# Kernel optimization log

Measured on AMD Instinct MI355X. Metric: run time of the kernel, lower is better.

The kernel has to match this reference:

```python
import jax, jax.numpy as jnp
import numpy as np
import math

EPS = 1e-8
NUM_FREQS = 64
NUM_BINS = 128
NUM_QUERIES = 32768
HEAD_DIM = NUM_FREQS * 2


def setup_inputs() -> dict:
    key = jax.random.key(0)
    k1, k2, k3, k4, k5 = jax.random.split(key, 5)
    init_value = math.log(math.e - 1.0)
    return {
        "Q": jax.random.normal(k1, (NUM_QUERIES, HEAD_DIM), dtype=jnp.float32),
        "rotated_probes": jax.random.normal(k2, (NUM_BINS, HEAD_DIM), dtype=jnp.float32),
        # faithful init is full(init_value); add small noise so grads are non-degenerate
        "q_weights_raw": init_value + 0.1 * jax.random.normal(k3, (NUM_BINS, NUM_FREQS), dtype=jnp.float32),
        "q_magnitude_weights": 0.1 * jax.random.normal(k4, (NUM_BINS, NUM_FREQS), dtype=jnp.float32),
        "q_bias": 0.1 * jax.random.normal(k5, (NUM_BINS,), dtype=jnp.float32),
    }


def reference(Q, rotated_probes, q_weights_raw, q_magnitude_weights, q_bias):
    F = NUM_FREQS
    # L2-normalize queries (use_l2_norm=True)
    Qn = Q / (jnp.linalg.norm(Q, axis=-1, keepdims=True) + EPS)  # (q, d)
    Q_real, Q_imag = Qn[:, :F], Qn[:, F:]                        # (q, f)
    P_real, P_imag = rotated_probes[:, :F], rotated_probes[:, F:]  # (b, f)
    # per-frequency complex error and distance: (q, b, f)
    error_real = P_real[None, :, :] - Q_real[:, None, :]
    error_imag = P_imag[None, :, :] - Q_imag[:, None, :]
    distance = jnp.sqrt(error_real ** 2 + error_imag ** 2 + EPS)
    # per-frequency magnitude of normalized Q: (q, f)
    Q_magnitude = jnp.sqrt(Q_real ** 2 + Q_imag ** 2 + EPS)
    # negative weights via softplus
    effective_weights = -jax.nn.softplus(q_weights_raw)          # (b, f)
    distance_term = jnp.einsum('qbf,bf->qb', distance, effective_weights)
    magnitude_term = Q_magnitude @ q_magnitude_weights.T          # (q, b)
    scores = distance_term + magnitude_term + q_bias[None, :]
    return scores
```

## Files before the change

### kernel.cpp

```cpp
#include <hip/hip_runtime.h>
#include <math.h>

#define NUM_FREQS   64
#define NUM_BINS    128
#define NUM_QUERIES 32768
#define HEAD_DIM    128
#define EPS         1e-8f
#define NQB         16

__global__ void prep_fused(const float* __restrict__ Q,
                           const float* __restrict__ rp,
                           const float* __restrict__ wraw,
                           const float* __restrict__ mw,
                           float2* __restrict__ Qri,
                           float*  __restrict__ Qm,
                           float4* __restrict__ probeA,
                           float*  __restrict__ probeM) {
    const int bid = blockIdx.x;
    const int tid = threadIdx.x;
    if (bid < 128) {
        int q = bid * 256 + tid;
        const float4* Qrow = reinterpret_cast<const float4*>(Q + (size_t)q * HEAD_DIM);
        float4 buf[32];
        float s = 0.0f;
        #pragma unroll
        for (int i = 0; i < 32; i++) {
            float4 v = Qrow[i];
            buf[i] = v;
            s = fmaf(v.x, v.x, fmaf(v.y, v.y, fmaf(v.z, v.z, fmaf(v.w, v.w, s))));
        }
        float inv = 1.0f / (__builtin_amdgcn_sqrtf(s) + EPS);
        #pragma unroll
        for (int i = 0; i < 16; i++) {
            float4 r  = buf[i];
            float4 im = buf[16 + i];
            float rr[4] = { r.x,  r.y,  r.z,  r.w  };
            float ii[4] = { im.x, im.y, im.z, im.w };
            #pragma unroll
            for (int k = 0; k < 4; k++) {
                float qr = rr[k] * inv;
                float qi = ii[k] * inv;
                float qm = __builtin_amdgcn_sqrtf(fmaf(qr, qr, fmaf(qi, qi, EPS)));
                int f = 4 * i + k;
                Qri[(size_t)f * NUM_QUERIES + q] = make_float2(qr, qi);
                Qm [(size_t)f * NUM_QUERIES + q] = qm;
            }
        }
    } else {
        int idx = (bid - 128) * 256 + tid;
        if (idx >= NUM_FREQS * NUM_BINS) return;
        int f = idx >> 7;
        int b = idx & 127;
        float pr = rp[b * HEAD_DIM + f];
        float pi = rp[b * HEAD_DIM + NUM_FREQS + f];
        float w  = wraw[b * NUM_FREQS + f];
        float sp = fmaxf(w, 0.0f) + log1pf(expf(-fabsf(w)));
        probeA[idx] = make_float4(-2.0f * pr, -2.0f * pi,
                                  fmaf(pr, pr, pi * pi), -sp);
        probeM[idx] = mw[b * NUM_FREQS + f];
    }
}

__global__ __launch_bounds__(256, 4) void main_kernel(
        const float4* __restrict__ probeA,
        const float*  __restrict__ probeM,
        const float2* __restrict__ Qri,
        const float*  __restrict__ Qm,
        const float*  __restrict__ bias,
        float*        __restrict__ out) {
    __shared__ float2 sri[NUM_FREQS + 1][NQB];
    __shared__ float  sqm[NUM_FREQS + 1][NQB];

    const int tid   = threadIdx.x;
    const int qbase = blockIdx.x * NQB;

    #pragma unroll
    for (int i = 0; i < 3; i++) {
        int idx = i * 256 + tid;
        if (idx < 512) {
            int f = idx >> 3, c = idx & 7;
            reinterpret_cast<float4*>(&sri[f][0])[c] =
                reinterpret_cast<const float4*>(Qri + (size_t)f * NUM_QUERIES + qbase)[c];
        } else {
            int t2 = idx - 512;
            int f = t2 >> 2, c = t2 & 3;
            reinterpret_cast<float4*>(&sqm[f][0])[c] =
                reinterpret_cast<const float4*>(Qm + (size_t)f * NUM_QUERIES + qbase)[c];
        }
    }
    __syncthreads();

    const int lane = tid & 63;
    const int wave = tid >> 6;
    const int jb   = wave * 4;

    float b0 = bias[lane];
    float b1 = bias[64 + lane];

    float acc0[4], acc1[4];
    #pragma unroll
    for (int p = 0; p < 4; p++) { acc0[p] = 0.0f; acc1[p] = 0.0f; }

    const float4* pA = probeA + lane;
    const float*  pM = probeM + lane;

    float4 P0  = pA[0];
    float4 P1  = pA[64];
    float  w0  = pM[0];
    float  w1  = pM[64];
    float4 r01 = *reinterpret_cast<const float4*>(&sri[0][jb]);
    float4 r23 = *reinterpret_cast<const float4*>(&sri[0][jb + 2]);
    float4 qm4 = *reinterpret_cast<const float4*>(&sqm[0][jb]);

    #pragma unroll 4
    for (int f = 0; f < NUM_FREQS; f++) {
        float4 r01n = *reinterpret_cast<const float4*>(&sri[f + 1][jb]);
        float4 r23n = *reinterpret_cast<const float4*>(&sri[f + 1][jb + 2]);
        float4 qm4n = *reinterpret_cast<const float4*>(&sqm[f + 1][jb]);
        pA += NUM_BINS; pM += NUM_BINS;
        float4 P0n = pA[0];
        float4 P1n = pA[64];
        float  w0n = pM[0];
        float  w1n = pM[64];
        __builtin_amdgcn_sched_barrier(0);

        const float qrv[4] = { r01.x, r01.z, r23.x, r23.z };
        const float qiv[4] = { r01.y, r01.w, r23.y, r23.w };
        const float qmv[4] = { qm4.x, qm4.y, qm4.z, qm4.w };

        #pragma unroll
        for (int p = 0; p < 4; p++) {
            float qr = qrv[p], qi = qiv[p], qm = qmv[p];
            {
                float a = fmaf(qm, qm, P0.z);
                a = fmaf(P0.x, qr, a);
                a = fmaf(P0.y, qi, a);
                float d = __builtin_amdgcn_sqrtf(a);
                acc0[p] = fmaf(d, P0.w, fmaf(qm, w0, acc0[p]));
            }
            {
                float a = fmaf(qm, qm, P1.z);
                a = fmaf(P1.x, qr, a);
                a = fmaf(P1.y, qi, a);
                float d = __builtin_amdgcn_sqrtf(a);
                acc1[p] = fmaf(d, P1.w, fmaf(qm, w1, acc1[p]));
            }
        }

        r01 = r01n; r23 = r23n; qm4 = qm4n;
        P0 = P0n; P1 = P1n; w0 = w0n; w1 = w1n;
    }

    #pragma unroll
    for (int p = 0; p < 4; p++) {
        size_t row = (size_t)(qbase + jb + p) * NUM_BINS;
        out[row + lane]      = acc0[p] + b0;
        out[row + 64 + lane] = acc1[p] + b1;
    }
}

__global__ void fallback_kernel(const float* __restrict__ Q,
                                const float* __restrict__ rp,
                                const float* __restrict__ wraw,
                                const float* __restrict__ mw,
                                const float* __restrict__ bias,
                                float* __restrict__ out) {
    __shared__ float qn[HEAD_DIM];
    __shared__ float qmag[NUM_FREQS];
    __shared__ float red[NUM_BINS];
    const int t = threadIdx.x;
    const int q = blockIdx.x;

    float v = Q[(size_t)q * HEAD_DIM + t];
    red[t] = v * v;
    __syncthreads();
    for (int s = 64; s > 0; s >>= 1) {
        if (t < s) red[t] += red[t + s];
        __syncthreads();
    }
    float inv = 1.0f / (__builtin_amdgcn_sqrtf(red[0]) + EPS);
    qn[t] = v * inv;
    __syncthreads();
    if (t < NUM_FREQS) {
        float a = qn[t], c = qn[t + NUM_FREQS];
        qmag[t] = __builtin_amdgcn_sqrtf(fmaf(a, a, fmaf(c, c, EPS)));
    }
    __syncthreads();

    const int b = t;
    float acc = 0.0f;
    for (int f = 0; f < NUM_FREQS; f++) {
        float pr = rp[(size_t)b * HEAD_DIM + f];
        float pi = rp[(size_t)b * HEAD_DIM + NUM_FREQS + f];
        float w  = wraw[(size_t)b * NUM_FREQS + f];
        float ew = -(fmaxf(w, 0.0f) + log1pf(expf(-fabsf(w))));
        float er = pr - qn[f];
        float ei = pi - qn[f + NUM_FREQS];
        float d  = __builtin_amdgcn_sqrtf(fmaf(er, er, fmaf(ei, ei, EPS)));
        acc = fmaf(d, ew, fmaf(qmag[f], mw[(size_t)b * NUM_FREQS + f], acc));
    }
    out[(size_t)q * NUM_BINS + b] = acc + bias[b];
}

extern "C" void kernel_launch(void* const* d_in, const int* in_sizes, int n_in,
                              void* d_out, int out_size, void* d_ws, size_t ws_size,
                              hipStream_t stream) {
    const float* Q    = (const float*)d_in[0];
    const float* rp   = (const float*)d_in[1];
    const float* wraw = (const float*)d_in[2];
    const float* mw   = (const float*)d_in[3];
    const float* bias = (const float*)d_in[4];
    float* out = (float*)d_out;

    const size_t pABytes  = (size_t)NUM_FREQS * NUM_BINS * sizeof(float4);
    const size_t pMBytes  = (size_t)NUM_FREQS * NUM_BINS * sizeof(float);
    const size_t qriBytes = (size_t)NUM_FREQS * NUM_QUERIES * sizeof(float2);
    const size_t qmBytes  = (size_t)NUM_FREQS * NUM_QUERIES * sizeof(float);
    const size_t need     = pABytes + pMBytes + qriBytes + qmBytes;

    if (ws_size >= need) {
        float4* probeA = (float4*)d_ws;
        float*  probeM = (float*)((char*)d_ws + pABytes);
        float2* Qri    = (float2*)((char*)d_ws + pABytes + pMBytes);
        float*  Qm     = (float*)((char*)d_ws + pABytes + pMBytes + qriBytes);

        hipLaunchKernelGGL(prep_fused, dim3(128 + 32), dim3(256), 0, stream,
                           Q, rp, wraw, mw, Qri, Qm, probeA, probeM);
        hipLaunchKernelGGL(main_kernel, dim3(NUM_QUERIES / NQB), dim3(256), 0,
                           stream, probeA, probeM, Qri, Qm, bias, out);
    } else {
        hipLaunchKernelGGL(fallback_kernel, dim3(NUM_QUERIES), dim3(NUM_BINS), 0,
                           stream, Q, rp, wraw, mw, bias, out);
    }
}
```

Measured before the change: 74.20 us.

## Fuse query normalization into main kernel, dropping transposed Q workspace

Query L2 normalization and per-frequency magnitude computation move from the prep kernel into the main kernel. Each block loads its 16 query rows directly, reduces the norm with wave shuffles, and writes the transposed real/imag and magnitude values into shared memory. This removes writing and re-reading the large frequency-major Qri/Qm workspace, a full round trip through global memory. The cost is an extra sync, some redundant shared-memory work per block, and scattered strided LDS stores.

```diff
diff --git a/kernel.cpp b/kernel.cpp
--- a/kernel.cpp
+++ b/kernel.cpp
@@ -8,64 +8,28 @@
 #define EPS         1e-8f
 #define NQB         16
 
-__global__ void prep_fused(const float* __restrict__ Q,
-                           const float* __restrict__ rp,
+__global__ void prep_probe(const float* __restrict__ rp,
                            const float* __restrict__ wraw,
                            const float* __restrict__ mw,
-                           float2* __restrict__ Qri,
-                           float*  __restrict__ Qm,
                            float4* __restrict__ probeA,
                            float*  __restrict__ probeM) {
-    const int bid = blockIdx.x;
-    const int tid = threadIdx.x;
-    if (bid < 128) {
-        int q = bid * 256 + tid;
-        const float4* Qrow = reinterpret_cast<const float4*>(Q + (size_t)q * HEAD_DIM);
-        float4 buf[32];
-        float s = 0.0f;
-        #pragma unroll
-        for (int i = 0; i < 32; i++) {
-            float4 v = Qrow[i];
-            buf[i] = v;
-            s = fmaf(v.x, v.x, fmaf(v.y, v.y, fmaf(v.z, v.z, fmaf(v.w, v.w, s))));
-        }
-        float inv = 1.0f / (__builtin_amdgcn_sqrtf(s) + EPS);
-        #pragma unroll
-        for (int i = 0; i < 16; i++) {
-            float4 r  = buf[i];
-            float4 im = buf[16 + i];
-            float rr[4] = { r.x,  r.y,  r.z,  r.w  };
-            float ii[4] = { im.x, im.y, im.z, im.w };
-            #pragma unroll
-            for (int k = 0; k < 4; k++) {
-                float qr = rr[k] * inv;
-                float qi = ii[k] * inv;
-                float qm = __builtin_amdgcn_sqrtf(fmaf(qr, qr, fmaf(qi, qi, EPS)));
-                int f = 4 * i + k;
-                Qri[(size_t)f * NUM_QUERIES + q] = make_float2(qr, qi);
-                Qm [(size_t)f * NUM_QUERIES + q] = qm;
-            }
-        }
-    } else {
-        int idx = (bid - 128) * 256 + tid;
-        if (idx >= NUM_FREQS * NUM_BINS) return;
-        int f = idx >> 7;
-        int b = idx & 127;
-        float pr = rp[b * HEAD_DIM + f];
-        float pi = rp[b * HEAD_DIM + NUM_FREQS + f];
-        float w  = wraw[b * NUM_FREQS + f];
-        float sp = fmaxf(w, 0.0f) + log1pf(expf(-fabsf(w)));
-        probeA[idx] = make_float4(-2.0f * pr, -2.0f * pi,
-                                  fmaf(pr, pr, pi * pi), -sp);
-        probeM[idx] = mw[b * NUM_FREQS + f];
-    }
+    int idx = blockIdx.x * 256 + threadIdx.x;
+    if (idx >= NUM_FREQS * NUM_BINS) return;
+    int f = idx >> 7;
+    int b = idx & 127;
+    float pr = rp[b * HEAD_DIM + f];
+    float pi = rp[b * HEAD_DIM + NUM_FREQS + f];
+    float w  = wraw[b * NUM_FREQS + f];
+    float sp = fmaxf(w, 0.0f) + log1pf(expf(-fabsf(w)));
+    probeA[idx] = make_float4(-2.0f * pr, -2.0f * pi,
+                              fmaf(pr, pr, pi * pi), -sp);
+    probeM[idx] = mw[b * NUM_FREQS + f];
 }
 
 __global__ __launch_bounds__(256, 4) void main_kernel(
         const float4* __restrict__ probeA,
         const float*  __restrict__ probeM,
-        const float2* __restrict__ Qri,
-        const float*  __restrict__ Qm,
+        const float*  __restrict__ Q,
         const float*  __restrict__ bias,
         float*        __restrict__ out) {
     __shared__ float2 sri[NUM_FREQS + 1][NQB];
@@ -74,19 +38,47 @@
     const int tid   = threadIdx.x;
     const int qbase = blockIdx.x * NQB;
 
+    {
+        const float4* Qb = reinterpret_cast<const float4*>(Q + (size_t)qbase * HEAD_DIM);
+        float4 v1 = Qb[tid];
+        float4 v2 = Qb[tid + 256];
+        const int c  = tid & 31;
+        const int r1 = tid >> 5;
+        const int r2 = r1 + 8;
+
+        float s1 = fmaf(v1.x, v1.x, fmaf(v1.y, v1.y, fmaf(v1.z, v1.z, v1.w * v1.w)));
+        float s2 = fmaf(v2.x, v2.x, fmaf(v2.y, v2.y, fmaf(v2.z, v2.z, v2.w * v2.w)));
+        #pragma unroll
+        for (int off = 1; off < 32; off <<= 1) {
+            s1 += __shfl_xor(s1, off);
+            s2 += __shfl_xor(s2, off);
+        }
+        float inv1 = 1.0f / (__builtin_amdgcn_sqrtf(s1) + EPS);
+        float inv2 = 1.0f / (__builtin_amdgcn_sqrtf(s2) + EPS);
+
+        const float a1[4] = { v1.x, v1.y, v1.z, v1.w };
+        const float a2[4] = { v2.x, v2.y, v2.z, v2.w };
+        #pragma unroll
+        for (int k = 0; k < 4; k++) {
+            int d = 4 * c + k;
+            float x1 = a1[k] * inv1;
+            float x2 = a2[k] * inv2;
+            if (d < NUM_FREQS) {
+                sri[d][r1].x = x1;
+                sri[d][r2].x = x2;
+            } else {
+                sri[d - NUM_FREQS][r1].y = x1;
+                sri[d - NUM_FREQS][r2].y = x2;
+            }
+        }
+    }
+    __syncthreads();
     #pragma unroll
-    for (int i = 0; i < 3; i++) {
-        int idx = i * 256 + tid;
-        if (idx < 512) {
-            int f = idx >> 3, c = idx & 7;
-            reinterpret_cast<float4*>(&sri[f][0])[c] =
-                reinterpret_cast<const float4*>(Qri + (size_t)f * NUM_QUERIES + qbase)[c];
-        } else {
-            int t2 = idx - 512;
-            int f = t2 >> 2, c = t2 & 3;
-            reinterpret_cast<float4*>(&sqm[f][0])[c] =
-                reinterpret_cast<const float4*>(Qm + (size_t)f * NUM_QUERIES + qbase)[c];
-        }
+    for (int i = 0; i < 4; i++) {
+        int e = i * 256 + tid;
+        int f = e >> 4, j = e & 15;
+        float2 ri = sri[f][j];
+        sqm[f][j] = __builtin_amdgcn_sqrtf(fmaf(ri.x, ri.x, fmaf(ri.y, ri.y, EPS)));
     }
     __syncthreads();
 
@@ -212,22 +204,18 @@
     const float* bias = (const float*)d_in[4];
     float* out = (float*)d_out;
 
-    const size_t pABytes  = (size_t)NUM_FREQS * NUM_BINS * sizeof(float4);
-    const size_t pMBytes  = (size_t)NUM_FREQS * NUM_BINS * sizeof(float);
-    const size_t qriBytes = (size_t)NUM_FREQS * NUM_QUERIES * sizeof(float2);
-    const size_t qmBytes  = (size_t)NUM_FREQS * NUM_QUERIES * sizeof(float);
-    const size_t need     = pABytes + pMBytes + qriBytes + qmBytes;
+    const size_t pABytes = (size_t)NUM_FREQS * NUM_BINS * sizeof(float4);
+    const size_t pMBytes = (size_t)NUM_FREQS * NUM_BINS * sizeof(float);
+    const size_t need    = pABytes + pMBytes + 4096;
 
     if (ws_size >= need) {
         float4* probeA = (float4*)d_ws;
         float*  probeM = (float*)((char*)d_ws + pABytes);
-        float2* Qri    = (float2*)((char*)d_ws + pABytes + pMBytes);
-        float*  Qm     = (float*)((char*)d_ws + pABytes + pMBytes + qriBytes);
-
-        hipLaunchKernelGGL(prep_fused, dim3(128 + 32), dim3(256), 0, stream,
-                           Q, rp, wraw, mw, Qri, Qm, probeA, probeM);
+
+        hipLaunchKernelGGL(prep_probe, dim3(32), dim3(256), 0, stream,
+                           rp, wraw, mw, probeA, probeM);
         hipLaunchKernelGGL(main_kernel, dim3(NUM_QUERIES / NQB), dim3(256), 0,
-                           stream, probeA, probeM, Qri, Qm, bias, out);
+                           stream, probeA, probeM, Q, bias, out);
     } else {
         hipLaunchKernelGGL(fallback_kernel, dim3(NUM_QUERIES), dim3(NUM_BINS), 0,
                            stream, Q, rp, wraw, mw, bias, out);
```

New measurement: 67.09 us. 1.11x faster.
